# Kernel tuning notes

Hardware: AMD Instinct MI355X
Metric: run time of the kernel (lower is better)

The kernel has to match this reference:

```python
import jax, jax.numpy as jnp
import numpy as np

N_NODES = 100000
N_EDGES = 1600000
IN_DIM = 128
HID_DIM = 64
OUT_DIM = 64


def setup_inputs() -> dict:
    key = jax.random.key(0)
    ks = jax.random.split(key, 8)
    x = jax.random.normal(ks[0], (N_NODES, IN_DIM), dtype=jnp.float32)
    edge_index = jax.random.randint(ks[1], (2, N_EDGES), 0, N_NODES, dtype=jnp.int64)
    edge_weight = jax.random.uniform(ks[2], (N_EDGES,), dtype=jnp.float32)  # cached PPMI values
    # Glorot-style params for the two PPMIConv layers
    W1 = jax.random.normal(ks[3], (IN_DIM, HID_DIM), dtype=jnp.float32) * (1.0 / np.sqrt(IN_DIM))
    b1 = jnp.zeros((HID_DIM,), dtype=jnp.float32)
    W2 = jax.random.normal(ks[4], (HID_DIM, OUT_DIM), dtype=jnp.float32) * (1.0 / np.sqrt(HID_DIM))
    b2 = jnp.zeros((OUT_DIM,), dtype=jnp.float32)
    return {"x": x, "edge_index": edge_index, "edge_weight": edge_weight,
            "W1": W1, "b1": b1, "W2": W2, "b2": b2}


def _gcn_norm(edge_index, edge_weight, num_nodes):
    # symmetric normalization of (PPMI) edge weights: D^{-1/2} A D^{-1/2}
    row, col = edge_index[0], edge_index[1]
    deg = jax.ops.segment_sum(edge_weight, row, num_segments=num_nodes)
    deg_inv_sqrt = jnp.where(deg > 0, jax.lax.rsqrt(jnp.maximum(deg, 1e-12)), 0.0)
    return deg_inv_sqrt[row] * edge_weight * deg_inv_sqrt[col]


def _ppmi_conv(x, W, b, edge_index, norm, num_nodes):
    h = x @ W                                   # [N, D_out] transform
    msg = h[edge_index[0]] * norm[:, None]      # [E, D_out] gather + weight
    out = jax.ops.segment_sum(msg, edge_index[1], num_segments=num_nodes)  # scatter-add
    return out + b


def reference(x, edge_index, edge_weight, W1, b1, W2, b2):
    n = x.shape[0]
    norm = _gcn_norm(edge_index, edge_weight, n)
    h = _ppmi_conv(x, W1, b1, edge_index, norm, n)
    h = jax.nn.relu(h)
    h = _ppmi_conv(h, W2, b2, edge_index, norm, n)
    return h
```

## Files before the change

### kernel.cpp

```cpp
#include <hip/hip_runtime.h>
#include <hip/hip_fp16.h>

#define N_NODES 100000
#define N_EDGES 1600000
#define IN_DIM 128
#define HID_DIM 64
#define OUT_DIM 64
#define NBKT 196
#define BSH 9
#define BMSK 511
#define NBLK 512
#define CHUNK 3125
#define MROW (NBKT * NBLK)

typedef _Float16 half8 __attribute__((ext_vector_type(8)));
typedef float f32x4 __attribute__((ext_vector_type(4)));

__global__ void count_kernel(const int* __restrict__ rows, const int* __restrict__ cols,
                             int* __restrict__ M) {
    __shared__ unsigned hc[NBKT], hr[NBKT];
    for (int i = threadIdx.x; i < NBKT; i += 256) { hc[i] = 0; hr[i] = 0; }
    __syncthreads();
    const int s = blockIdx.x * CHUNK;
    const int e = min(s + CHUNK, N_EDGES);
    for (int i = s + threadIdx.x; i < e; i += 256) {
        atomicAdd(&hr[rows[i] >> BSH], 1u);
        atomicAdd(&hc[cols[i] >> BSH], 1u);
    }
    __syncthreads();
    for (int i = threadIdx.x; i < NBKT; i += 256) {
        M[i * NBLK + blockIdx.x] = (int)hc[i];
        M[MROW + i * NBLK + blockIdx.x] = (int)hr[i];
    }
}

__global__ void block_sum_kernel(const int* __restrict__ counts, int* __restrict__ partials, int n) {
    __shared__ int sh[256];
    int base = blockIdx.x * 1024;
    int s = 0;
    for (int i = threadIdx.x; i < 1024; i += 256) {
        int idx = base + i;
        s += (idx < n) ? counts[idx] : 0;
    }
    sh[threadIdx.x] = s;
    __syncthreads();
    for (int off = 128; off > 0; off >>= 1) {
        if (threadIdx.x < off) sh[threadIdx.x] += sh[threadIdx.x + off];
        __syncthreads();
    }
    if (threadIdx.x == 0) partials[blockIdx.x] = sh[0];
}

__global__ void scan_partials_kernel(int* __restrict__ p, int nb) {
    __shared__ int sh[256];
    int t = threadIdx.x;
    int v = (t < nb) ? p[t] : 0;
    sh[t] = v;
    __syncthreads();
    for (int off = 1; off < 256; off <<= 1) {
        int add = (t >= off) ? sh[t - off] : 0;
        __syncthreads();
        sh[t] += add;
        __syncthreads();
    }
    if (t < nb) p[t] = sh[t] - v;
}

__global__ void scan_final_kernel(const int* __restrict__ counts, const int* __restrict__ partials,
                                  int* __restrict__ offsets, int n) {
    __shared__ int sh[256];
    int t = threadIdx.x;
    int idx0 = blockIdx.x * 1024 + t * 4;
    int v[4];
    int s = 0;
#pragma unroll
    for (int j = 0; j < 4; ++j) {
        int id = idx0 + j;
        v[j] = (id < n) ? counts[id] : 0;
        s += v[j];
    }
    sh[t] = s;
    __syncthreads();
    for (int off = 1; off < 256; off <<= 1) {
        int add = (t >= off) ? sh[t - off] : 0;
        __syncthreads();
        sh[t] += add;
        __syncthreads();
    }
    int run = sh[t] - s + partials[blockIdx.x];
#pragma unroll
    for (int j = 0; j < 4; ++j) {
        int id = idx0 + j;
        if (id < n) offsets[id] = run;
        run += v[j];
    }
    if (idx0 <= n - 1 && n - 1 < idx0 + 4) offsets[n] = run;
}

__global__ void scatter_kernel(const int* __restrict__ rows, const int* __restrict__ cols,
                               const float* __restrict__ w, const int* __restrict__ Ms,
                               unsigned long long* __restrict__ pk) {
    __shared__ unsigned curC[NBKT], curR[NBKT];
    for (int i = threadIdx.x; i < NBKT; i += 256) {
        curC[i] = (unsigned)Ms[i * NBLK + blockIdx.x];
        curR[i] = (unsigned)Ms[MROW + i * NBLK + blockIdx.x];
    }
    __syncthreads();
    const int s = blockIdx.x * CHUNK;
    const int e = min(s + CHUNK, N_EDGES);
    for (int i = s + threadIdx.x; i < e; i += 256) {
        int r = rows[i], c = cols[i];
        unsigned wb = __float_as_uint(w[i]);
        unsigned pA = atomicAdd(&curC[c >> BSH], 1u);
        pk[pA] = ((unsigned long long)wb << 32) | (unsigned)(((c & BMSK) << 17) | r);
        unsigned pR = atomicAdd(&curR[r >> BSH], 1u);
        pk[pR] = ((unsigned long long)wb << 32) | (unsigned)(r & BMSK);
    }
}

__global__ void deg_reduce_kernel(const unsigned long long* __restrict__ pk,
                                  const int* __restrict__ Ms, float* __restrict__ dis) {
    __shared__ float acc[512];
    const int b = blockIdx.x;
    const int t = threadIdx.x;
    acc[t] = 0.f; acc[t + 256] = 0.f;
    __syncthreads();
    const int s = Ms[MROW + b * NBLK];
    const int e = Ms[MROW + (b + 1) * NBLK];
    for (int i = s + t; i < e; i += 256) {
        unsigned long long p = pk[i];
        atomicAdd(&acc[(unsigned)p & (unsigned)BMSK], __uint_as_float((unsigned)(p >> 32)));
    }
    __syncthreads();
#pragma unroll
    for (int k = 0; k < 2; ++k) {
        int node = b * 512 + t + k * 256;
        if (node < N_NODES) {
            float d = acc[t + k * 256];
            dis[node] = d > 0.f ? rsqrtf(fmaxf(d, 1e-12f)) : 0.f;
        }
    }
}

__global__ void fill_kernel(const unsigned long long* __restrict__ pk,
                            const int* __restrict__ Ms, const float* __restrict__ dis,
                            int2* __restrict__ csr, int* __restrict__ offsets) {
    __shared__ unsigned hist[512];
    __shared__ unsigned pairs[256];
    const int b = blockIdx.x;
    const int t = threadIdx.x;
    hist[t] = 0; hist[t + 256] = 0;
    __syncthreads();
    const int s = Ms[b * NBLK];
    const int e = Ms[(b + 1) * NBLK];
    for (int i = s + t; i < e; i += 256) {
        unsigned lo = (unsigned)pk[i];
        atomicAdd(&hist[(lo >> 17) & (unsigned)BMSK], 1u);
    }
    __syncthreads();
    unsigned h0 = hist[2 * t], h1 = hist[2 * t + 1];
    pairs[t] = h0 + h1;
    __syncthreads();
    for (int off = 1; off < 256; off <<= 1) {
        unsigned add = (t >= off) ? pairs[t - off] : 0;
        __syncthreads();
        pairs[t] += add;
        __syncthreads();
    }
    unsigned P = pairs[t] - (h0 + h1) + (unsigned)s;
    unsigned e0 = P, e1 = P + h0;
    int n0 = b * 512 + 2 * t;
    int n1 = n0 + 1;
    if (n0 <= N_NODES) offsets[n0] = (int)e0;
    if (n1 <= N_NODES) offsets[n1] = (int)e1;
    hist[2 * t] = e0; hist[2 * t + 1] = e1;
    __syncthreads();
    for (int i = s + t; i < e; i += 256) {
        unsigned long long p = pk[i];
        unsigned lo = (unsigned)p;
        unsigned cl = (lo >> 17) & (unsigned)BMSK;
        int r = (int)(lo & 0x1FFFFu);
        unsigned pos = atomicAdd(&hist[cl], 1u);
        int c = (b << BSH) + (int)cl;
        float nv = dis[r] * __uint_as_float((unsigned)(p >> 32)) * dis[c];
        csr[pos] = make_int2(r, __float_as_int(nv));
    }
}

__global__ void wfrag_kernel(const float* __restrict__ W1, const float* __restrict__ W2,
                             __half* __restrict__ F1, __half* __restrict__ F2) {
    int t = blockIdx.x * 256 + threadIdx.x;
    if (t < 1024) {
        int lane = t & 63, fg = t >> 6;
        int col = (fg & 3) * 16 + (lane & 15);
        int kb = (fg >> 2) * 32 + (lane >> 4) * 8;
        __half v[8];
#pragma unroll
        for (int j = 0; j < 8; ++j) v[j] = __float2half(W1[(kb + j) * 64 + col]);
        *reinterpret_cast<uint4*>(F1 + (size_t)t * 8) = *reinterpret_cast<uint4*>(v);
    } else if (t < 1536) {
        int u = t - 1024;
        int lane = u & 63, fg = u >> 6;
        int col = (fg & 3) * 16 + (lane & 15);
        int kb = (fg >> 2) * 32 + (lane >> 4) * 8;
        __half v[8];
#pragma unroll
        for (int j = 0; j < 8; ++j) v[j] = __float2half(W2[(kb + j) * 64 + col]);
        *reinterpret_cast<uint4*>(F2 + (size_t)u * 8) = *reinterpret_cast<uint4*>(v);
    }
}

__global__ __launch_bounds__(256) void gemm1_mfma(
        const float* __restrict__ x, const __half* __restrict__ F1, __half* __restrict__ h1) {
    const int wid = threadIdx.x >> 6, lane = threadIdx.x & 63;
    const int row0 = blockIdx.x * 64 + wid * 16;
    int arow = min(row0 + (lane & 15), N_NODES - 1);
    const int kb0 = (lane >> 4) * 8;
    const float* ap = x + (size_t)arow * 128 + kb0;

    f32x4 acc[4] = {};
#pragma unroll
    for (int c = 0; c < 4; ++c) {
        float4 a0 = *reinterpret_cast<const float4*>(ap + c * 32);
        float4 a1 = *reinterpret_cast<const float4*>(ap + c * 32 + 4);
        half8 af;
        af[0] = (_Float16)a0.x; af[1] = (_Float16)a0.y; af[2] = (_Float16)a0.z; af[3] = (_Float16)a0.w;
        af[4] = (_Float16)a1.x; af[5] = (_Float16)a1.y; af[6] = (_Float16)a1.z; af[7] = (_Float16)a1.w;
#pragma unroll
        for (int ct = 0; ct < 4; ++ct) {
            half8 bf = *reinterpret_cast<const half8*>(F1 + ((size_t)(c * 4 + ct) * 64 + lane) * 8);
            acc[ct] = __builtin_amdgcn_mfma_f32_16x16x32_f16(af, bf, acc[ct], 0, 0, 0);
        }
    }
    const int prow = row0 + ((lane >> 4) << 2);
    const int col = lane & 15;
#pragma unroll
    for (int ct = 0; ct < 4; ++ct)
#pragma unroll
        for (int r = 0; r < 4; ++r) {
            int rr = prow + r;
            if (rr < N_NODES) h1[(size_t)rr * 64 + ct * 16 + col] = __float2half(acc[ct][r]);
        }
}

__global__ __launch_bounds__(256) void gemm2_mfma(
        const __half* __restrict__ g, const __half* __restrict__ F2,
        const float* __restrict__ b2, float* __restrict__ out) {
    const int wid = threadIdx.x >> 6, lane = threadIdx.x & 63;
    const int row0 = blockIdx.x * 64 + wid * 16;
    int arow = min(row0 + (lane & 15), N_NODES - 1);
    const int kb0 = (lane >> 4) * 8;
    const __half* ap = g + (size_t)arow * 64 + kb0;

    f32x4 acc[4] = {};
#pragma unroll
    for (int c = 0; c < 2; ++c) {
        half8 af = *reinterpret_cast<const half8*>(ap + c * 32);
#pragma unroll
        for (int ct = 0; ct < 4; ++ct) {
            half8 bf = *reinterpret_cast<const half8*>(F2 + ((size_t)(c * 4 + ct) * 64 + lane) * 8);
            acc[ct] = __builtin_amdgcn_mfma_f32_16x16x32_f16(af, bf, acc[ct], 0, 0, 0);
        }
    }
    const int prow = row0 + ((lane >> 4) << 2);
    const int col = lane & 15;
#pragma unroll
    for (int ct = 0; ct < 4; ++ct) {
        float bb = b2[ct * 16 + col];
#pragma unroll
        for (int r = 0; r < 4; ++r) {
            int rr = prow + r;
            if (rr < N_NODES) out[(size_t)rr * 64 + ct * 16 + col] = acc[ct][r] + bb;
        }
    }
}

template <int BIAS_RELU>
__global__ __launch_bounds__(512) void gather_vec_kernel(
        const __half* __restrict__ h, const int2* __restrict__ csr,
        const int* __restrict__ offsets, const float* __restrict__ bias,
        __half* __restrict__ outh, int n) {
    int node = blockIdx.x * 8 + (threadIdx.x >> 6);
    int lane = threadIdx.x & 63;
    int q = lane & 7;
    int g = lane >> 3;
    int s = offsets[node];
    int e = offsets[node + 1];

    float a0 = 0.f, a1 = 0.f, a2 = 0.f, a3 = 0.f, a4 = 0.f, a5 = 0.f, a6 = 0.f, a7 = 0.f;
    for (int j = s; j < e; j += 16) {
        int eA = j + g;
        int eB = j + 8 + g;
        int2 pA = csr[min(eA, e - 1)];
        int2 pB = csr[min(eB, e - 1)];
        float nA = (eA < e) ? __int_as_float(pA.y) : 0.f;
        float nB = (eB < e) ? __int_as_float(pB.y) : 0.f;
        uint4 uA = *reinterpret_cast<const uint4*>(h + ((size_t)pA.x << 6) + (q << 3));
        uint4 uB = *reinterpret_cast<const uint4*>(h + ((size_t)pB.x << 6) + (q << 3));
        float2 f;
        f = __half22float2(__builtin_bit_cast(__half2, uA.x)); a0 = fmaf(f.x, nA, a0); a1 = fmaf(f.y, nA, a1);
        f = __half22float2(__builtin_bit_cast(__half2, uA.y)); a2 = fmaf(f.x, nA, a2); a3 = fmaf(f.y, nA, a3);
        f = __half22float2(__builtin_bit_cast(__half2, uA.z)); a4 = fmaf(f.x, nA, a4); a5 = fmaf(f.y, nA, a5);
        f = __half22float2(__builtin_bit_cast(__half2, uA.w)); a6 = fmaf(f.x, nA, a6); a7 = fmaf(f.y, nA, a7);
        f = __half22float2(__builtin_bit_cast(__half2, uB.x)); a0 = fmaf(f.x, nB, a0); a1 = fmaf(f.y, nB, a1);
        f = __half22float2(__builtin_bit_cast(__half2, uB.y)); a2 = fmaf(f.x, nB, a2); a3 = fmaf(f.y, nB, a3);
        f = __half22float2(__builtin_bit_cast(__half2, uB.z)); a4 = fmaf(f.x, nB, a4); a5 = fmaf(f.y, nB, a5);
        f = __half22float2(__builtin_bit_cast(__half2, uB.w)); a6 = fmaf(f.x, nB, a6); a7 = fmaf(f.y, nB, a7);
    }
#pragma unroll
    for (int m = 8; m <= 32; m <<= 1) {
        a0 += __shfl_xor(a0, m); a1 += __shfl_xor(a1, m);
        a2 += __shfl_xor(a2, m); a3 += __shfl_xor(a3, m);
        a4 += __shfl_xor(a4, m); a5 += __shfl_xor(a5, m);
        a6 += __shfl_xor(a6, m); a7 += __shfl_xor(a7, m);
    }
    if (BIAS_RELU) {
        const float4 b0 = *reinterpret_cast<const float4*>(bias + (q << 3));
        const float4 b1 = *reinterpret_cast<const float4*>(bias + (q << 3) + 4);
        a0 = fmaxf(a0 + b0.x, 0.f); a1 = fmaxf(a1 + b0.y, 0.f);
        a2 = fmaxf(a2 + b0.z, 0.f); a3 = fmaxf(a3 + b0.w, 0.f);
        a4 = fmaxf(a4 + b1.x, 0.f); a5 = fmaxf(a5 + b1.y, 0.f);
        a6 = fmaxf(a6 + b1.z, 0.f); a7 = fmaxf(a7 + b1.w, 0.f);
    }
    if (g == 0) {
        __half2 o0 = __float22half2_rn(make_float2(a0, a1));
        __half2 o1 = __float22half2_rn(make_float2(a2, a3));
        __half2 o2 = __float22half2_rn(make_float2(a4, a5));
        __half2 o3 = __float22half2_rn(make_float2(a6, a7));
        uint4 u = make_uint4(__builtin_bit_cast(unsigned, o0), __builtin_bit_cast(unsigned, o1),
                             __builtin_bit_cast(unsigned, o2), __builtin_bit_cast(unsigned, o3));
        *reinterpret_cast<uint4*>(outh + ((size_t)node << 6) + (q << 3)) = u;
    }
}

extern "C" void kernel_launch(void* const* d_in, const int* in_sizes, int n_in,
                              void* d_out, int out_size, void* d_ws, size_t ws_size,
                              hipStream_t stream) {
    const float* x  = (const float*)d_in[0];
    const int*   ei = (const int*)d_in[1];
    const float* ew = (const float*)d_in[2];
    const float* W1 = (const float*)d_in[3];
    const float* b1 = (const float*)d_in[4];
    const float* W2 = (const float*)d_in[5];
    const float* b2 = (const float*)d_in[6];
    float* out = (float*)d_out;
    char*  ws  = (char*)d_ws;

    const int* rows = ei;
    const int* cols = ei + N_EDGES;

    int2*     csr      = (int2*)(ws + 0);
    unsigned long long* pk = (unsigned long long*)(ws + 12800000);
    __half*   h1       = (__half*)(ws + 12800000);
    __half*   g        = (__half*)(ws + 12800000);
    __half*   t        = (__half*)(ws + 25600000);
    int*      M        = (int*)(ws + 38400000);
    int*      Ms       = (int*)(ws + 39202816);
    int*      partials = (int*)(ws + 40005636);
    int*      offsets  = (int*)(ws + 40006424);
    float*    dis      = (float*)(ws + 40406428);
    __half*   F1       = (__half*)(ws + 40806432);
    __half*   F2       = (__half*)(ws + 40822816);

    const int TPB = 256;
    const int n2  = 2 * MROW;
    const int nSB2 = (n2 + 1023) / 1024;

    wfrag_kernel<<<6, TPB, 0, stream>>>(W1, W2, F1, F2);

    count_kernel<<<NBLK, TPB, 0, stream>>>(rows, cols, M);

    block_sum_kernel<<<nSB2, 256, 0, stream>>>(M, partials, n2);
    scan_partials_kernel<<<1, 256, 0, stream>>>(partials, nSB2);
    scan_final_kernel<<<nSB2, 256, 0, stream>>>(M, partials, Ms, n2);

    scatter_kernel<<<NBLK, TPB, 0, stream>>>(rows, cols, ew, Ms, pk);

    deg_reduce_kernel<<<NBKT, TPB, 0, stream>>>(pk, Ms, dis);

    fill_kernel<<<NBKT, TPB, 0, stream>>>(pk, Ms, dis, csr, offsets);

    gemm1_mfma<<<(N_NODES + 63) / 64, TPB, 0, stream>>>(x, F1, h1);

    gather_vec_kernel<1><<<N_NODES / 8, 512, 0, stream>>>(h1, csr, offsets, b1, t, N_NODES);

    gather_vec_kernel<0><<<N_NODES / 8, 512, 0, stream>>>(t, csr, offsets, b1, g, N_NODES);

    gemm2_mfma<<<(N_NODES + 63) / 64, TPB, 0, stream>>>(g, F2, b2, out);
}
```

Baseline: 199.8 us.

## Stage scatter through LDS and fold degree normalization into GEMM and gather epilogues

The scatter kernel now sorts each chunk of edges by bucket in shared memory and then writes them out contiguously, which replaces the old scattered global stores. The row-side degree payload is shrunk to 32 bits, with the weight stored as fp16. The D^{-1/2} factors are no longer applied per edge in fill. Instead they are applied per node: in the gemm1 epilogue and in the gather epilogues (scaling before and after the bias/relu). This removes two random dis gathers per edge, at the cost of fp16 precision in the degree sums and extra shared-memory use in scatter, which lowers its occupancy.

New measurement: 193.8 us. 3.0% less time.

```diff
diff --git a/kernel.cpp b/kernel.cpp
--- a/kernel.cpp
+++ b/kernel.cpp
@@ -97,39 +97,91 @@
     if (idx0 <= n - 1 && n - 1 < idx0 + 4) offsets[n] = run;
 }
 
-__global__ void scatter_kernel(const int* __restrict__ rows, const int* __restrict__ cols,
-                               const float* __restrict__ w, const int* __restrict__ Ms,
-                               unsigned long long* __restrict__ pk) {
-    __shared__ unsigned curC[NBKT], curR[NBKT];
-    for (int i = threadIdx.x; i < NBKT; i += 256) {
-        curC[i] = (unsigned)Ms[i * NBLK + blockIdx.x];
-        curR[i] = (unsigned)Ms[MROW + i * NBLK + blockIdx.x];
-    }
-    __syncthreads();
-    const int s = blockIdx.x * CHUNK;
-    const int e = min(s + CHUNK, N_EDGES);
-    for (int i = s + threadIdx.x; i < e; i += 256) {
+__global__ __launch_bounds__(256) void scatter_kernel(
+        const int* __restrict__ rows, const int* __restrict__ cols,
+        const float* __restrict__ w, const int* __restrict__ M, const int* __restrict__ Ms,
+        unsigned long long* __restrict__ pkA, unsigned* __restrict__ pkR) {
+    __shared__ unsigned long long pay[CHUNK];
+    __shared__ unsigned char bkt[CHUNK + 3];
+    __shared__ unsigned scn[256];
+    __shared__ unsigned base[NBKT], cur[NBKT], gbase[NBKT];
+    const int blk = blockIdx.x, t = threadIdx.x;
+    const int s = blk * CHUNK;
+
+    unsigned cnt = (t < NBKT) ? (unsigned)M[t * NBLK + blk] : 0;
+    scn[t] = cnt;
+    __syncthreads();
+    for (int off = 1; off < 256; off <<= 1) {
+        unsigned a = (t >= off) ? scn[t - off] : 0;
+        __syncthreads();
+        scn[t] += a;
+        __syncthreads();
+    }
+    if (t < NBKT) {
+        unsigned b0 = scn[t] - cnt;
+        base[t] = b0; cur[t] = b0;
+        gbase[t] = (unsigned)Ms[t * NBLK + blk];
+    }
+    __syncthreads();
+    for (int i = s + t; i < s + CHUNK; i += 256) {
         int r = rows[i], c = cols[i];
-        unsigned wb = __float_as_uint(w[i]);
-        unsigned pA = atomicAdd(&curC[c >> BSH], 1u);
-        pk[pA] = ((unsigned long long)wb << 32) | (unsigned)(((c & BMSK) << 17) | r);
-        unsigned pR = atomicAdd(&curR[r >> BSH], 1u);
-        pk[pR] = ((unsigned long long)wb << 32) | (unsigned)(r & BMSK);
-    }
-}
-
-__global__ void deg_reduce_kernel(const unsigned long long* __restrict__ pk,
+        unsigned b = (unsigned)c >> BSH;
+        unsigned p = atomicAdd(&cur[b], 1u);
+        pay[p] = ((unsigned long long)__float_as_uint(w[i]) << 32) |
+                 (unsigned)(((c & BMSK) << 17) | r);
+        bkt[p] = (unsigned char)b;
+    }
+    __syncthreads();
+    for (int i = t; i < CHUNK; i += 256) {
+        unsigned b = bkt[i];
+        pkA[gbase[b] + (i - base[b])] = pay[i];
+    }
+    __syncthreads();
+
+    cnt = (t < NBKT) ? (unsigned)M[MROW + t * NBLK + blk] : 0;
+    scn[t] = cnt;
+    __syncthreads();
+    for (int off = 1; off < 256; off <<= 1) {
+        unsigned a = (t >= off) ? scn[t - off] : 0;
+        __syncthreads();
+        scn[t] += a;
+        __syncthreads();
+    }
+    if (t < NBKT) {
+        unsigned b0 = scn[t] - cnt;
+        base[t] = b0; cur[t] = b0;
+        gbase[t] = (unsigned)Ms[MROW + t * NBLK + blk] - (unsigned)N_EDGES;
+    }
+    __syncthreads();
+    unsigned* pay32 = (unsigned*)pay;
+    for (int i = s + t; i < s + CHUNK; i += 256) {
+        int r = rows[i];
+        unsigned b = (unsigned)r >> BSH;
+        unsigned p = atomicAdd(&cur[b], 1u);
+        unsigned short hw = __half_as_ushort(__float2half(w[i]));
+        pay32[p] = ((unsigned)hw << 16) | (unsigned)(r & BMSK);
+        bkt[p] = (unsigned char)b;
+    }
+    __syncthreads();
+    for (int i = t; i < CHUNK; i += 256) {
+        unsigned b = bkt[i];
+        pkR[gbase[b] + (i - base[b])] = pay32[i];
+    }
+}
+
+__global__ void deg_reduce_kernel(const unsigned* __restrict__ pkR,
                                   const int* __restrict__ Ms, float* __restrict__ dis) {
     __shared__ float acc[512];
     const int b = blockIdx.x;
     const int t = threadIdx.x;
     acc[t] = 0.f; acc[t + 256] = 0.f;
     __syncthreads();
-    const int s = Ms[MROW + b * NBLK];
-    const int e = Ms[MROW + (b + 1) * NBLK];
+    const int s = Ms[MROW + b * NBLK] - N_EDGES;
+    const int e = Ms[MROW + (b + 1) * NBLK] - N_EDGES;
     for (int i = s + t; i < e; i += 256) {
-        unsigned long long p = pk[i];
-        atomicAdd(&acc[(unsigned)p & (unsigned)BMSK], __uint_as_float((unsigned)(p >> 32)));
+        unsigned u = pkR[i];
+        float wv = __half2float(__ushort_as_half((unsigned short)(u >> 16)));
+        atomicAdd(&acc[u & (unsigned)BMSK], wv);
     }
     __syncthreads();
 #pragma unroll
@@ -143,7 +195,7 @@
 }
 
 __global__ void fill_kernel(const unsigned long long* __restrict__ pk,
-                            const int* __restrict__ Ms, const float* __restrict__ dis,
+                            const int* __restrict__ Ms,
                             int2* __restrict__ csr, int* __restrict__ offsets) {
     __shared__ unsigned hist[512];
     __shared__ unsigned pairs[256];
@@ -181,9 +233,7 @@
         unsigned cl = (lo >> 17) & (unsigned)BMSK;
         int r = (int)(lo & 0x1FFFFu);
         unsigned pos = atomicAdd(&hist[cl], 1u);
-        int c = (b << BSH) + (int)cl;
-        float nv = dis[r] * __uint_as_float((unsigned)(p >> 32)) * dis[c];
-        csr[pos] = make_int2(r, __float_as_int(nv));
+        csr[pos] = make_int2(r, (int)(unsigned)(p >> 32));
     }
 }
 
@@ -211,7 +261,8 @@
 }
 
 __global__ __launch_bounds__(256) void gemm1_mfma(
-        const float* __restrict__ x, const __half* __restrict__ F1, __half* __restrict__ h1) {
+        const float* __restrict__ x, const __half* __restrict__ F1,
+        const float* __restrict__ dis, __half* __restrict__ h1) {
     const int wid = threadIdx.x >> 6, lane = threadIdx.x & 63;
     const int row0 = blockIdx.x * 64 + wid * 16;
     int arow = min(row0 + (lane & 15), N_NODES - 1);
@@ -235,12 +286,15 @@
     const int prow = row0 + ((lane >> 4) << 2);
     const int col = lane & 15;
 #pragma unroll
-    for (int ct = 0; ct < 4; ++ct)
-#pragma unroll
-        for (int r = 0; r < 4; ++r) {
-            int rr = prow + r;
-            if (rr < N_NODES) h1[(size_t)rr * 64 + ct * 16 + col] = __float2half(acc[ct][r]);
-        }
+    for (int r = 0; r < 4; ++r) {
+        int rr = prow + r;
+        if (rr < N_NODES) {
+            float dv = dis[rr];
+#pragma unroll
+            for (int ct = 0; ct < 4; ++ct)
+                h1[(size_t)rr * 64 + ct * 16 + col] = __float2half(acc[ct][r] * dv);
+        }
+    }
 }
 
 __global__ __launch_bounds__(256) void gemm2_mfma(
@@ -279,7 +333,7 @@
 __global__ __launch_bounds__(512) void gather_vec_kernel(
         const __half* __restrict__ h, const int2* __restrict__ csr,
         const int* __restrict__ offsets, const float* __restrict__ bias,
-        __half* __restrict__ outh, int n) {
+        const float* __restrict__ dis, __half* __restrict__ outh, int n) {
     int node = blockIdx.x * 8 + (threadIdx.x >> 6);
     int lane = threadIdx.x & 63;
     int q = lane & 7;
@@ -314,15 +368,19 @@
         a4 += __shfl_xor(a4, m); a5 += __shfl_xor(a5, m);
         a6 += __shfl_xor(a6, m); a7 += __shfl_xor(a7, m);
     }
-    if (BIAS_RELU) {
-        const float4 b0 = *reinterpret_cast<const float4*>(bias + (q << 3));
-        const float4 b1 = *reinterpret_cast<const float4*>(bias + (q << 3) + 4);
-        a0 = fmaxf(a0 + b0.x, 0.f); a1 = fmaxf(a1 + b0.y, 0.f);
-        a2 = fmaxf(a2 + b0.z, 0.f); a3 = fmaxf(a3 + b0.w, 0.f);
-        a4 = fmaxf(a4 + b1.x, 0.f); a5 = fmaxf(a5 + b1.y, 0.f);
-        a6 = fmaxf(a6 + b1.z, 0.f); a7 = fmaxf(a7 + b1.w, 0.f);
-    }
     if (g == 0) {
+        float dv = dis[node];
+        if (BIAS_RELU) {
+            const float4 b0 = *reinterpret_cast<const float4*>(bias + (q << 3));
+            const float4 b1 = *reinterpret_cast<const float4*>(bias + (q << 3) + 4);
+            a0 = fmaxf(fmaf(a0, dv, b0.x), 0.f) * dv; a1 = fmaxf(fmaf(a1, dv, b0.y), 0.f) * dv;
+            a2 = fmaxf(fmaf(a2, dv, b0.z), 0.f) * dv; a3 = fmaxf(fmaf(a3, dv, b0.w), 0.f) * dv;
+            a4 = fmaxf(fmaf(a4, dv, b1.x), 0.f) * dv; a5 = fmaxf(fmaf(a5, dv, b1.y), 0.f) * dv;
+            a6 = fmaxf(fmaf(a6, dv, b1.z), 0.f) * dv; a7 = fmaxf(fmaf(a7, dv, b1.w), 0.f) * dv;
+        } else {
+            a0 *= dv; a1 *= dv; a2 *= dv; a3 *= dv;
+            a4 *= dv; a5 *= dv; a6 *= dv; a7 *= dv;
+        }
         __half2 o0 = __float22half2_rn(make_float2(a0, a1));
         __half2 o1 = __float22half2_rn(make_float2(a2, a3));
         __half2 o2 = __float22half2_rn(make_float2(a4, a5));
@@ -350,7 +408,8 @@
     const int* cols = ei + N_EDGES;
 
     int2*     csr      = (int2*)(ws + 0);
-    unsigned long long* pk = (unsigned long long*)(ws + 12800000);
+    unsigned long long* pkA = (unsigned long long*)(ws + 12800000);
+    unsigned* pkR      = (unsigned*)(ws + 25600000);
     __half*   h1       = (__half*)(ws + 12800000);
     __half*   g        = (__half*)(ws + 12800000);
     __half*   t        = (__half*)(ws + 25600000);
@@ -374,17 +433,17 @@
     scan_partials_kernel<<<1, 256, 0, stream>>>(partials, nSB2);
     scan_final_kernel<<<nSB2, 256, 0, stream>>>(M, partials, Ms, n2);
 
-    scatter_kernel<<<NBLK, TPB, 0, stream>>>(rows, cols, ew, Ms, pk);
-
-    deg_reduce_kernel<<<NBKT, TPB, 0, stream>>>(pk, Ms, dis);
-
-    fill_kernel<<<NBKT, TPB, 0, stream>>>(pk, Ms, dis, csr, offsets);
-
-    gemm1_mfma<<<(N_NODES + 63) / 64, TPB, 0, stream>>>(x, F1, h1);
-
-    gather_vec_kernel<1><<<N_NODES / 8, 512, 0, stream>>>(h1, csr, offsets, b1, t, N_NODES);
-
-    gather_vec_kernel<0><<<N_NODES / 8, 512, 0, stream>>>(t, csr, offsets, b1, g, N_NODES);
+    scatter_kernel<<<NBLK, TPB, 0, stream>>>(rows, cols, ew, M, Ms, pkA, pkR);
+
+    deg_reduce_kernel<<<NBKT, TPB, 0, stream>>>(pkR, Ms, dis);
+
+    fill_kernel<<<NBKT, TPB, 0, stream>>>(pkA, Ms, csr, offsets);
+
+    gemm1_mfma<<<(N_NODES + 63) / 64, TPB, 0, stream>>>(x, F1, dis, h1);
+
+    gather_vec_kernel<1><<<N_NODES / 8, 512, 0, stream>>>(h1, csr, offsets, b1, dis, t, N_NODES);
+
+    gather_vec_kernel<0><<<N_NODES / 8, 512, 0, stream>>>(t, csr, offsets, b1, dis, g, N_NODES);
 
     gemm2_mfma<<<(N_NODES + 63) / 64, TPB, 0, stream>>>(g, F2, b2, out);
 }
```
